# Optimization experiments

Hardware: AMD Instinct MI355X
Metric: run time of the kernel (lower is better)

The kernel has to match this reference:

```python
import jax, jax.numpy as jnp
import numpy as np

N_NODES = 100000
N_EDGES = 1600000
IN_FEATS = 128
HEADS = 4
OUT_FEATS = 32
NEG_SLOPE = 0.2


def setup_inputs() -> dict:
    key = jax.random.key(0)
    ks = jax.random.split(key, 7)
    x = jax.random.normal(ks[0], (N_NODES, IN_FEATS), dtype=jnp.float32)
    fc_w = jax.random.normal(ks[1], (HEADS * OUT_FEATS, IN_FEATS), dtype=jnp.float32) * (1.0 / np.sqrt(IN_FEATS))
    attn_l = jax.random.normal(ks[2], (HEADS, OUT_FEATS), dtype=jnp.float32) * (1.0 / np.sqrt(OUT_FEATS))
    attn_r = jax.random.normal(ks[3], (HEADS, OUT_FEATS), dtype=jnp.float32) * (1.0 / np.sqrt(OUT_FEATS))
    bias = jnp.zeros((HEADS * OUT_FEATS,), dtype=jnp.float32)
    src = jax.random.randint(ks[4], (N_EDGES,), 0, N_NODES, dtype=jnp.int64 if jax.config.jax_enable_x64 else jnp.int32)
    dst = jax.random.randint(ks[5], (N_EDGES,), 0, N_NODES, dtype=jnp.int64 if jax.config.jax_enable_x64 else jnp.int32)
    return {"x": x, "fc_w": fc_w, "attn_l": attn_l, "attn_r": attn_r, "bias": bias, "src": src, "dst": dst}


def reference(x, fc_w, attn_l, attn_r, bias, src, dst):
    """DGL GATConv (feat_drop=attn_drop=0, residual identity since in==H*D,
    allow_zero_in_degree=True, activation=None), then concat heads."""
    N = x.shape[0]
    H, D = attn_l.shape
    # linear projection: [N, H, D]
    feat = (x @ fc_w.T).reshape(N, H, D)
    # per-node attention halves: [N, H]
    el = jnp.einsum('nhd,hd->nh', feat, attn_l)
    er = jnp.einsum('nhd,hd->nh', feat, attn_r)
    # per-edge score with leaky relu: [E, H]
    e = el[src] + er[dst]
    e = jnp.where(e > 0, e, NEG_SLOPE * e)
    # edge softmax grouped by destination node
    emax = jax.ops.segment_max(e, dst, num_segments=N)          # [N, H]
    ee = jnp.exp(e - emax[dst])                                  # [E, H]
    denom = jax.ops.segment_sum(ee, dst, num_segments=N)        # [N, H]
    a = ee / jnp.maximum(denom[dst], jnp.float32(1e-38))         # [E, H]
    # weighted message + scatter aggregate: [N, H, D]
    msg = feat[src] * a[:, :, None]
    rst = jax.ops.segment_sum(msg, dst, num_segments=N)
    # residual (identity since in_feats == H*D) + bias
    rst = rst + x.reshape(N, H, D) + bias.reshape(1, H, D)
    # concat heads
    return rst.reshape(N, H * D)
```

## Files before the change

kernel.cpp:

```cpp
#include <hip/hip_runtime.h>
#include <math.h>

#define NEG_SLOPE 0.2f
#define PB 256
#define BKT_SHIFT 8
#define WSLICES 8

typedef __attribute__((ext_vector_type(8))) short bf16x8;
typedef __attribute__((ext_vector_type(4))) float f32x4;

__device__ __forceinline__ unsigned bf16_rne(float f) {
  unsigned u = __float_as_uint(f);
  return (u + 0x7fff + ((u >> 16) & 1)) >> 16;
}

__device__ __forceinline__ float lrelu_exp(float v) {
  v = v > 0.f ? v : NEG_SLOPE * v;
  return __expf(v);
}

__global__ void fc_conv(const float* __restrict__ fc_w,
                        unsigned* __restrict__ fc_wb, int n) {
  const int i = blockIdx.x * 256 + threadIdx.x;
  if (i < n) {
    const float2 v = reinterpret_cast<const float2*>(fc_w)[i];
    fc_wb[i] = bf16_rne(v.x) | (bf16_rne(v.y) << 16);
  }
}

__global__ __launch_bounds__(256) void gemm_feat_attn(
    const float* __restrict__ x, const unsigned* __restrict__ fc_wb,
    const float* __restrict__ attn_l, const float* __restrict__ attn_r,
    unsigned* __restrict__ featb, float* __restrict__ el,
    float* __restrict__ er, int N)
{
  __shared__ __align__(16) unsigned x_lds[64 * 68];
  __shared__ __align__(16) unsigned w_lds[128 * 68];
  const int t = threadIdx.x;
  const int row_base = blockIdx.x * 64;

  {
    const uint4* fb4 = reinterpret_cast<const uint4*>(fc_wb);
#pragma unroll
    for (int k = 0; k < 8; ++k) {
      const int i4 = t + k * 256;
      const uint4 v = fb4[i4];
      const int row = i4 >> 4;
      unsigned* d = &w_lds[row * 68 + (i4 & 15) * 4];
      d[0] = v.x; d[1] = v.y; d[2] = v.z; d[3] = v.w;
    }
  }
  {
    const int r = t >> 2, q = t & 3;
    const int grow = min(row_base + r, N - 1);
    const float* src = x + (size_t)grow * 128 + q * 32;
    unsigned* dstp = &x_lds[r * 68 + q * 16];
#pragma unroll
    for (int i = 0; i < 8; ++i) {
      const float4 v = *reinterpret_cast<const float4*>(src + i * 4);
      dstp[2 * i]     = bf16_rne(v.x) | (bf16_rne(v.y) << 16);
      dstp[2 * i + 1] = bf16_rne(v.z) | (bf16_rne(v.w) << 16);
    }
  }
  __syncthreads();

  const int w = t >> 6;
  const int l = t & 63;
  const int cl = l & 15;
  const int g = l >> 4;

  bf16x8 a_frag[4];
#pragma unroll
  for (int ks = 0; ks < 4; ++ks)
    a_frag[ks] = *reinterpret_cast<const bf16x8*>(
        &x_lds[(w * 16 + cl) * 68 + ks * 16 + g * 4]);

  f32x4 acc[8];
#pragma unroll
  for (int ct = 0; ct < 8; ++ct) acc[ct] = (f32x4){0.f, 0.f, 0.f, 0.f};

#pragma unroll
  for (int ct = 0; ct < 8; ++ct) {
#pragma unroll
    for (int ks = 0; ks < 4; ++ks) {
      const bf16x8 b_frag = *reinterpret_cast<const bf16x8*>(
          &w_lds[(ct * 16 + cl) * 68 + ks * 16 + g * 4]);
      acc[ct] = __builtin_amdgcn_mfma_f32_16x16x32_bf16(a_frag[ks], b_frag,
                                                        acc[ct], 0, 0, 0);
    }
  }

#pragma unroll
  for (int ct = 0; ct < 8; ++ct) {
#pragma unroll
    for (int r = 0; r < 4; ++r) {
      const float v = acc[ct][r];
      const float vn = __shfl_xor(v, 1);
      const int node = row_base + w * 16 + g * 4 + r;
      if ((cl & 1) == 0 && node < N) {
        featb[(size_t)node * 64 + ct * 8 + (cl >> 1)] =
            bf16_rne(v) | (bf16_rne(vn) << 16);
      }
    }
  }

  float al_lo[4], al_hi[4], ar_lo[4], ar_hi[4];
#pragma unroll
  for (int h = 0; h < 4; ++h) {
    al_lo[h] = attn_l[h * 32 + cl];
    al_hi[h] = attn_l[h * 32 + 16 + cl];
    ar_lo[h] = attn_r[h * 32 + cl];
    ar_hi[h] = attn_r[h * 32 + 16 + cl];
  }
#pragma unroll
  for (int r = 0; r < 4; ++r) {
    const int node = row_base + w * 16 + g * 4 + r;
#pragma unroll
    for (int h = 0; h < 4; ++h) {
      float pl = acc[2 * h][r] * al_lo[h] + acc[2 * h + 1][r] * al_hi[h];
      float pr = acc[2 * h][r] * ar_lo[h] + acc[2 * h + 1][r] * ar_hi[h];
#pragma unroll
      for (int d = 1; d < 16; d <<= 1) {
        pl += __shfl_xor(pl, d);
        pr += __shfl_xor(pr, d);
      }
      if (cl == 0 && node < N) {
        el[(size_t)node * 4 + h] = pl;
        er[(size_t)node * 4 + h] = pr;
      }
    }
  }
}

__global__ __launch_bounds__(256) void hist_bucket(const int* __restrict__ dst,
                                                   int* __restrict__ hist,
                                                   int E, int NB, int chunk) {
  __shared__ int h[512];
  const int k = blockIdx.x, t = threadIdx.x;
  for (int i = t; i < NB; i += 256) h[i] = 0;
  __syncthreads();
  const int beg = k * chunk, end = min(E, beg + chunk);
  for (int e = beg + t; e < end; e += 256)
    atomicAdd(&h[dst[e] >> BKT_SHIFT], 1);
  __syncthreads();
  for (int i = t; i < NB; i += 256) hist[i * PB + k] = h[i];
}

__global__ __launch_bounds__(256) void scan_a(const int* __restrict__ deg,
                                              int* __restrict__ offs,
                                              int* __restrict__ blk_sums,
                                              int n) {
  __shared__ int wsum[4];
  const int b = blockIdx.x, t = threadIdx.x;
  const int base = b * 2048 + t * 8;
  int v[8];
  int s = 0;
#pragma unroll
  for (int j = 0; j < 8; ++j) {
    v[j] = s;
    const int d = (base + j < n) ? deg[base + j] : 0;
    s += d;
  }
  const int lane = t & 63;
  int incl = s;
#pragma unroll
  for (int d = 1; d < 64; d <<= 1) {
    const int o = __shfl_up(incl, d);
    if (lane >= d) incl += o;
  }
  const int w = t >> 6;
  if (lane == 63) wsum[w] = incl;
  __syncthreads();
  int woff = 0;
  for (int ww = 0; ww < w; ++ww) woff += wsum[ww];
  const int thr_excl = woff + incl - s;
#pragma unroll
  for (int j = 0; j < 8; ++j)
    if (base + j < n) offs[base + j] = thr_excl + v[j];
  if (t == 255) blk_sums[b] = woff + incl;
}

__global__ void scan_b(const int* __restrict__ blk_sums,
                       int* __restrict__ blk_off, int* __restrict__ offs,
                       int n, int nb) {
  const int lane = threadIdx.x & 63;
  int v = (lane < nb) ? blk_sums[lane] : 0;
  int incl = v;
#pragma unroll
  for (int d = 1; d < 64; d <<= 1) {
    const int o = __shfl_up(incl, d);
    if (lane >= d) incl += o;
  }
  if (lane < nb) blk_off[lane] = incl - v;
  if (lane == 63) offs[n] = incl;
}

__global__ __launch_bounds__(256) void part_scatter(
    const int* __restrict__ src, const int* __restrict__ dst,
    const int* __restrict__ hscan, const int* __restrict__ blk_off,
    unsigned* __restrict__ part, int E, int NB, int chunk) {
  __shared__ int cur[512];
  const int k = blockIdx.x, t = threadIdx.x;
  for (int i = t; i < NB; i += 256) {
    const int m = i * PB + k;
    cur[i] = hscan[m] + blk_off[m >> 11];
  }
  __syncthreads();
  const int beg = k * chunk, end = min(E, beg + chunk);
  for (int e = beg + t; e < end; e += 256) {
    const int d = dst[e];
    const int b = d >> BKT_SHIFT;
    const int pos = atomicAdd(&cur[b], 1);
    part[pos] = (unsigned)src[e] |
                ((unsigned)(d & ((1 << BKT_SHIFT) - 1)) << 20);
  }
}

__global__ __launch_bounds__(256) void build_csr(
    const unsigned* __restrict__ part, const int* __restrict__ hscan,
    const int* __restrict__ blk_off, int* __restrict__ node_offs,
    unsigned* __restrict__ csr, int N, int E, int NB) {
  __shared__ int cnt[256];
  __shared__ int wtot[4];
  const int b = blockIdx.x, t = threadIdx.x;
  const int m0 = b * PB;
  const int bbase = hscan[m0] + blk_off[m0 >> 11];
  int bend = E;
  if (b + 1 < NB) {
    const int m1 = (b + 1) * PB;
    bend = hscan[m1] + blk_off[m1 >> 11];
  }
  const int node0 = b << BKT_SHIFT;
  cnt[t] = 0;
  __syncthreads();
  for (int p = bbase + t; p < bend; p += 256)
    atomicAdd(&cnt[part[p] >> 20], 1);
  __syncthreads();
  const int a0 = cnt[t];
  int incl = a0;
#pragma unroll
  for (int d1 = 1; d1 < 64; d1 <<= 1) {
    const int o = __shfl_up(incl, d1);
    if ((t & 63) >= d1) incl += o;
  }
  const int w = t >> 6;
  if ((t & 63) == 63) wtot[w] = incl;
  __syncthreads();
  int woff = 0;
  for (int ww = 0; ww < w; ++ww) woff += wtot[ww];
  const int e0 = woff + incl - a0;
  cnt[t] = e0;
  if (node0 + t < N) node_offs[node0 + t] = bbase + e0;
  if (b == NB - 1 && t == 0) node_offs[N] = E;
  __syncthreads();
  for (int p = bbase + t; p < bend; p += 256) {
    const unsigned v = part[p];
    const int lpos = atomicAdd(&cnt[v >> 20], 1);
    csr[bbase + lpos] = v;
  }
}

__global__ __launch_bounds__(256) void compute_w(
    const unsigned* __restrict__ csr, const int* __restrict__ hscan,
    const int* __restrict__ blk_off, const float* __restrict__ el,
    const float* __restrict__ er, float4* __restrict__ wsb, int E, int NB) {
  const int b = blockIdx.x / WSLICES;
  const int sl = blockIdx.x - b * WSLICES;
  const int m0 = b * PB;
  const int bbase = hscan[m0] + blk_off[m0 >> 11];
  int bend = E;
  if (b + 1 < NB) {
    const int m1 = (b + 1) * PB;
    bend = hscan[m1] + blk_off[m1 >> 11];
  }
  const int node0 = b << BKT_SHIFT;
  const int len = bend - bbase;
  const int per = (len + WSLICES - 1) / WSLICES;
  const int s0 = bbase + sl * per;
  const int s1 = min(bend, s0 + per);
  for (int pos = s0 + (int)threadIdx.x; pos < s1; pos += 256) {
    const unsigned v = csr[pos];
    const unsigned s = v & 0xFFFFFu;
    const unsigned ld = v >> 20;
    const float4 l4 = *reinterpret_cast<const float4*>(el + s * 4);
    const float4 r4 =
        *reinterpret_cast<const float4*>(er + (unsigned)(node0 + ld) * 4);
    float4 wv;
    wv.x = lrelu_exp(l4.x + r4.x);
    wv.y = lrelu_exp(l4.y + r4.y);
    wv.z = lrelu_exp(l4.z + r4.z);
    wv.w = lrelu_exp(l4.w + r4.w);
    wsb[pos] = wv;
  }
}

__global__ __launch_bounds__(256) void agg_kernel(
    const uint2* __restrict__ featb2, const unsigned* __restrict__ csr,
    const float* __restrict__ wf, const float* __restrict__ x,
    const float* __restrict__ bias, const int* __restrict__ node_offs,
    float* __restrict__ out, int N, int E)
{
  const int n = (int)((blockIdx.x * (size_t)blockDim.x + threadIdx.x) >> 6);
  if (n >= N) return;
  const unsigned lane = threadIdx.x & 63;
  const unsigned half = lane >> 5;
  const unsigned li = lane & 31;
  const unsigned hh = li >> 3;
  const int beg = node_offs[n];
  const int end = node_offs[n + 1];
  const int nfull = (end - beg) >> 3;

  float a0 = 0.f, a1 = 0.f, a2 = 0.f, a3 = 0.f, ds = 0.f;
  int p = beg;
  for (int gi = 0; gi < nfull; ++gi, p += 8) {
    unsigned pk[4]; float wv[4]; uint2 fv[4];
#pragma unroll
    for (int i = 0; i < 4; ++i) pk[i] = csr[(unsigned)p + 2 * i + half];
#pragma unroll
    for (int i = 0; i < 4; ++i)
      wv[i] = wf[((unsigned)p + 2 * i + half) * 4 + hh];
#pragma unroll
    for (int i = 0; i < 4; ++i)
      fv[i] = featb2[(pk[i] & 0xFFFFFu) * 32 + li];
#pragma unroll
    for (int i = 0; i < 4; ++i) {
      a0 = fmaf(wv[i], __uint_as_float(fv[i].x << 16), a0);
      a1 = fmaf(wv[i], __uint_as_float(fv[i].x & 0xffff0000u), a1);
      a2 = fmaf(wv[i], __uint_as_float(fv[i].y << 16), a2);
      a3 = fmaf(wv[i], __uint_as_float(fv[i].y & 0xffff0000u), a3);
      ds += wv[i];
    }
  }
  if (p < end) {
    const int last = end - 1;
#pragma unroll
    for (int i = 0; i < 4; ++i) {
      const int e = p + 2 * i + (int)half;
      const unsigned ec = (unsigned)min(e, last);
      const unsigned pk = csr[ec];
      float w = wf[ec * 4 + hh];
      if (e > last) w = 0.f;
      const uint2 fv = featb2[(pk & 0xFFFFFu) * 32 + li];
      a0 = fmaf(w, __uint_as_float(fv.x << 16), a0);
      a1 = fmaf(w, __uint_as_float(fv.x & 0xffff0000u), a1);
      a2 = fmaf(w, __uint_as_float(fv.y << 16), a2);
      a3 = fmaf(w, __uint_as_float(fv.y & 0xffff0000u), a3);
      ds += w;
    }
  }

  a0 += __shfl_xor(a0, 32);
  a1 += __shfl_xor(a1, 32);
  a2 += __shfl_xor(a2, 32);
  a3 += __shfl_xor(a3, 32);
  ds += __shfl_xor(ds, 32);

  if (half == 0) {
    const float inv = 1.f / fmaxf(ds, 1e-38f);
    const float4 xr = ((const float4*)x)[(unsigned)n * 32 + li];
    const float4 br = ((const float4*)bias)[li];
    float4 o;
    o.x = fmaf(a0, inv, xr.x + br.x);
    o.y = fmaf(a1, inv, xr.y + br.y);
    o.z = fmaf(a2, inv, xr.z + br.z);
    o.w = fmaf(a3, inv, xr.w + br.w);
    ((float4*)out)[(unsigned)n * 32 + li] = o;
  }
}

extern "C" void kernel_launch(void* const* d_in, const int* in_sizes, int n_in,
                              void* d_out, int out_size, void* d_ws,
                              size_t ws_size, hipStream_t stream) {
  const float* x      = (const float*)d_in[0];
  const float* fc_w   = (const float*)d_in[1];
  const float* attn_l = (const float*)d_in[2];
  const float* attn_r = (const float*)d_in[3];
  const float* bias   = (const float*)d_in[4];
  const int*   src    = (const int*)d_in[5];
  const int*   dst    = (const int*)d_in[6];
  const int N = in_sizes[0] / 128;
  const int E = in_sizes[5];
  float* out = (float*)d_out;

  const int NB = (N + 255) >> 8;
  const int M = NB * PB;
  const int chunk = (E + PB - 1) / PB;

  char* ws = (char*)d_ws;
  size_t off = 0;
  auto alloc = [&](size_t bytes) {
    void* p = ws + off;
    off += (bytes + 255) & ~(size_t)255;
    return p;
  };
  unsigned* featb   = (unsigned*)alloc((size_t)N * 128 * 2);
  unsigned* fc_wb   = (unsigned*)alloc(128 * 64 * 4);
  float* el         = (float*)alloc((size_t)N * 4 * 4);
  float* er         = (float*)alloc((size_t)N * 4 * 4);
  int*   hist       = (int*)alloc((size_t)M * 4);
  int*   hscan      = (int*)alloc((size_t)(M + 1) * 4);
  int*   node_offs  = (int*)alloc((size_t)(N + 1) * 4);
  int*   blk_sums   = (int*)alloc(256);
  int*   blk_off    = (int*)alloc(256);
  unsigned* part    = (unsigned*)alloc((size_t)E * 4);
  unsigned* csr     = (unsigned*)alloc((size_t)E * 4);
  float4* wsb       = (float4*)alloc((size_t)E * 16);

  fc_conv<<<32, 256, 0, stream>>>(fc_w, fc_wb, 128 * 64);
  gemm_feat_attn<<<(N + 63) / 64, 256, 0, stream>>>(x, fc_wb, attn_l, attn_r,
                                                    featb, el, er, N);
  hist_bucket<<<PB, 256, 0, stream>>>(dst, hist, E, NB, chunk);
  const int nb = (M + 2047) / 2048;
  scan_a<<<nb, 256, 0, stream>>>(hist, hscan, blk_sums, M);
  scan_b<<<1, 64, 0, stream>>>(blk_sums, blk_off, hscan, M, nb);
  part_scatter<<<PB, 256, 0, stream>>>(src, dst, hscan, blk_off, part, E, NB,
                                       chunk);
  build_csr<<<NB, 256, 0, stream>>>(part, hscan, blk_off, node_offs, csr, N,
                                    E, NB);
  compute_w<<<NB * WSLICES, 256, 0, stream>>>(csr, hscan, blk_off, el, er,
                                              wsb, E, NB);
  agg_kernel<<<(N + 3) / 4, 256, 0, stream>>>((const uint2*)featb, csr,
                                              (const float*)wsb, x, bias,
                                              node_offs, out, N, E);
}
```

Before: 170.1 us.

## Fold weight conversion into histogram, load GEMM A directly, unroll aggregation deeper

Folds the fc_w bf16 conversion into the hist_bucket kernel, which removes one kernel launch; hist_bucket now runs before the GEMM. The GEMM loads and converts its x fragments straight from global memory into registers, dropping the x LDS staging buffer, which lowers LDS use and may allow higher occupancy. The aggregation loop now processes 16 edges per iteration instead of 8, giving more gathers in flight, and the tail is restructured to match. In exchange it uses more registers, and short neighbour lists spend more of their work in the masked tail.

Result: faster. 163.1 us (-4.1%).

```diff
diff --git a/kernel.cpp b/kernel.cpp
--- a/kernel.cpp
+++ b/kernel.cpp
@@ -17,15 +17,6 @@
 __device__ __forceinline__ float lrelu_exp(float v) {
   v = v > 0.f ? v : NEG_SLOPE * v;
   return __expf(v);
-}
-
-__global__ void fc_conv(const float* __restrict__ fc_w,
-                        unsigned* __restrict__ fc_wb, int n) {
-  const int i = blockIdx.x * 256 + threadIdx.x;
-  if (i < n) {
-    const float2 v = reinterpret_cast<const float2*>(fc_w)[i];
-    fc_wb[i] = bf16_rne(v.x) | (bf16_rne(v.y) << 16);
-  }
 }
 
 __global__ __launch_bounds__(256) void gemm_feat_attn(
@@ -34,7 +25,6 @@
     unsigned* __restrict__ featb, float* __restrict__ el,
     float* __restrict__ er, int N)
 {
-  __shared__ __align__(16) unsigned x_lds[64 * 68];
   __shared__ __align__(16) unsigned w_lds[128 * 68];
   const int t = threadIdx.x;
   const int row_base = blockIdx.x * 64;
@@ -50,30 +40,28 @@
       d[0] = v.x; d[1] = v.y; d[2] = v.z; d[3] = v.w;
     }
   }
-  {
-    const int r = t >> 2, q = t & 3;
-    const int grow = min(row_base + r, N - 1);
-    const float* src = x + (size_t)grow * 128 + q * 32;
-    unsigned* dstp = &x_lds[r * 68 + q * 16];
-#pragma unroll
-    for (int i = 0; i < 8; ++i) {
-      const float4 v = *reinterpret_cast<const float4*>(src + i * 4);
-      dstp[2 * i]     = bf16_rne(v.x) | (bf16_rne(v.y) << 16);
-      dstp[2 * i + 1] = bf16_rne(v.z) | (bf16_rne(v.w) << 16);
-    }
-  }
-  __syncthreads();
 
   const int w = t >> 6;
   const int l = t & 63;
   const int cl = l & 15;
   const int g = l >> 4;
 
+  const int arow = min(row_base + w * 16 + cl, N - 1);
+  const float* __restrict__ xp = x + (size_t)arow * 128;
   bf16x8 a_frag[4];
 #pragma unroll
-  for (int ks = 0; ks < 4; ++ks)
-    a_frag[ks] = *reinterpret_cast<const bf16x8*>(
-        &x_lds[(w * 16 + cl) * 68 + ks * 16 + g * 4]);
+  for (int ks = 0; ks < 4; ++ks) {
+    const float4 v0 = *reinterpret_cast<const float4*>(xp + ks * 32 + g * 8);
+    const float4 v1 =
+        *reinterpret_cast<const float4*>(xp + ks * 32 + g * 8 + 4);
+    uint4 uu;
+    uu.x = bf16_rne(v0.x) | (bf16_rne(v0.y) << 16);
+    uu.y = bf16_rne(v0.z) | (bf16_rne(v0.w) << 16);
+    uu.z = bf16_rne(v1.x) | (bf16_rne(v1.y) << 16);
+    uu.w = bf16_rne(v1.z) | (bf16_rne(v1.w) << 16);
+    a_frag[ks] = *reinterpret_cast<bf16x8*>(&uu);
+  }
+  __syncthreads();
 
   f32x4 acc[8];
 #pragma unroll
@@ -134,9 +122,16 @@
 
 __global__ __launch_bounds__(256) void hist_bucket(const int* __restrict__ dst,
                                                    int* __restrict__ hist,
+                                                   const float* __restrict__ fc_w,
+                                                   unsigned* __restrict__ fc_wb,
                                                    int E, int NB, int chunk) {
   __shared__ int h[512];
   const int k = blockIdx.x, t = threadIdx.x;
+  if (k < 32) {
+    const int i = k * 256 + t;
+    const float2 v = reinterpret_cast<const float2*>(fc_w)[i];
+    fc_wb[i] = bf16_rne(v.x) | (bf16_rne(v.y) << 16);
+  }
   for (int i = t; i < NB; i += 256) h[i] = 0;
   __syncthreads();
   const int beg = k * chunk, end = min(E, beg + chunk);
@@ -308,22 +303,22 @@
   const unsigned hh = li >> 3;
   const int beg = node_offs[n];
   const int end = node_offs[n + 1];
-  const int nfull = (end - beg) >> 3;
+  const int nfull = (end - beg) >> 4;
 
   float a0 = 0.f, a1 = 0.f, a2 = 0.f, a3 = 0.f, ds = 0.f;
   int p = beg;
-  for (int gi = 0; gi < nfull; ++gi, p += 8) {
-    unsigned pk[4]; float wv[4]; uint2 fv[4];
-#pragma unroll
-    for (int i = 0; i < 4; ++i) pk[i] = csr[(unsigned)p + 2 * i + half];
-#pragma unroll
-    for (int i = 0; i < 4; ++i)
+  for (int gi = 0; gi < nfull; ++gi, p += 16) {
+    unsigned pk[8]; float wv[8]; uint2 fv[8];
+#pragma unroll
+    for (int i = 0; i < 8; ++i) pk[i] = csr[(unsigned)p + 2 * i + half];
+#pragma unroll
+    for (int i = 0; i < 8; ++i)
       wv[i] = wf[((unsigned)p + 2 * i + half) * 4 + hh];
 #pragma unroll
-    for (int i = 0; i < 4; ++i)
+    for (int i = 0; i < 8; ++i)
       fv[i] = featb2[(pk[i] & 0xFFFFFu) * 32 + li];
 #pragma unroll
-    for (int i = 0; i < 4; ++i) {
+    for (int i = 0; i < 8; ++i) {
       a0 = fmaf(wv[i], __uint_as_float(fv[i].x << 16), a0);
       a1 = fmaf(wv[i], __uint_as_float(fv[i].x & 0xffff0000u), a1);
       a2 = fmaf(wv[i], __uint_as_float(fv[i].y << 16), a2);
@@ -333,19 +328,25 @@
   }
   if (p < end) {
     const int last = end - 1;
-#pragma unroll
-    for (int i = 0; i < 4; ++i) {
-      const int e = p + 2 * i + (int)half;
-      const unsigned ec = (unsigned)min(e, last);
-      const unsigned pk = csr[ec];
-      float w = wf[ec * 4 + hh];
-      if (e > last) w = 0.f;
-      const uint2 fv = featb2[(pk & 0xFFFFFu) * 32 + li];
-      a0 = fmaf(w, __uint_as_float(fv.x << 16), a0);
-      a1 = fmaf(w, __uint_as_float(fv.x & 0xffff0000u), a1);
-      a2 = fmaf(w, __uint_as_float(fv.y << 16), a2);
-      a3 = fmaf(w, __uint_as_float(fv.y & 0xffff0000u), a3);
-      ds += w;
+    unsigned pk[8]; float wv[8]; uint2 fv[8]; int ee[8];
+#pragma unroll
+    for (int i = 0; i < 8; ++i) ee[i] = p + 2 * i + (int)half;
+#pragma unroll
+    for (int i = 0; i < 8; ++i) pk[i] = csr[(unsigned)min(ee[i], last)];
+#pragma unroll
+    for (int i = 0; i < 8; ++i)
+      wv[i] = wf[(unsigned)min(ee[i], last) * 4 + hh];
+#pragma unroll
+    for (int i = 0; i < 8; ++i)
+      fv[i] = featb2[(pk[i] & 0xFFFFFu) * 32 + li];
+#pragma unroll
+    for (int i = 0; i < 8; ++i) {
+      if (ee[i] > last) wv[i] = 0.f;
+      a0 = fmaf(wv[i], __uint_as_float(fv[i].x << 16), a0);
+      a1 = fmaf(wv[i], __uint_as_float(fv[i].x & 0xffff0000u), a1);
+      a2 = fmaf(wv[i], __uint_as_float(fv[i].y << 16), a2);
+      a3 = fmaf(wv[i], __uint_as_float(fv[i].y & 0xffff0000u), a3);
+      ds += wv[i];
     }
   }
 
@@ -406,10 +407,9 @@
   unsigned* csr     = (unsigned*)alloc((size_t)E * 4);
   float4* wsb       = (float4*)alloc((size_t)E * 16);
 
-  fc_conv<<<32, 256, 0, stream>>>(fc_w, fc_wb, 128 * 64);
+  hist_bucket<<<PB, 256, 0, stream>>>(dst, hist, fc_w, fc_wb, E, NB, chunk);
   gemm_feat_attn<<<(N + 63) / 64, 256, 0, stream>>>(x, fc_wb, attn_l, attn_r,
                                                     featb, el, er, N);
-  hist_bucket<<<PB, 256, 0, stream>>>(dst, hist, E, NB, chunk);
   const int nb = (M + 2047) / 2048;
   scan_a<<<nb, 256, 0, stream>>>(hist, hscan, blk_sums, M);
   scan_b<<<1, 64, 0, stream>>>(blk_sums, blk_off, hscan, M, nb);
```

## Fuse weight computation into CSR build, store bf16 weights, drop extra kernels

Applied to the files above, without the earlier changes.

Edge-weight computation moves into build_csr, which now uses 512 threads and writes bf16-packed weights next to the scatter, so the compute_w pass and its re-read of csr are gone. The fc_w bf16 conversion is folded into hist_bucket, and gemm reads x straight from global into MFMA fragments instead of staging it in LDS. agg_kernel reads 2-byte weights instead of 4-byte ones, halving that traffic. The cost is lower weight precision, and the fused scatter does its el/er gathers while holding the atomic path, which may reduce occupancy.

Measured after the change: 168.4 us. About the same (-1.0%).

```diff
diff --git a/kernel.cpp b/kernel.cpp
--- a/kernel.cpp
+++ b/kernel.cpp
@@ -4,7 +4,6 @@
 #define NEG_SLOPE 0.2f
 #define PB 256
 #define BKT_SHIFT 8
-#define WSLICES 8
 
 typedef __attribute__((ext_vector_type(8))) short bf16x8;
 typedef __attribute__((ext_vector_type(4))) float f32x4;
@@ -17,15 +16,6 @@
 __device__ __forceinline__ float lrelu_exp(float v) {
   v = v > 0.f ? v : NEG_SLOPE * v;
   return __expf(v);
-}
-
-__global__ void fc_conv(const float* __restrict__ fc_w,
-                        unsigned* __restrict__ fc_wb, int n) {
-  const int i = blockIdx.x * 256 + threadIdx.x;
-  if (i < n) {
-    const float2 v = reinterpret_cast<const float2*>(fc_w)[i];
-    fc_wb[i] = bf16_rne(v.x) | (bf16_rne(v.y) << 16);
-  }
 }
 
 __global__ __launch_bounds__(256) void gemm_feat_attn(
@@ -34,7 +24,6 @@
     unsigned* __restrict__ featb, float* __restrict__ el,
     float* __restrict__ er, int N)
 {
-  __shared__ __align__(16) unsigned x_lds[64 * 68];
   __shared__ __align__(16) unsigned w_lds[128 * 68];
   const int t = threadIdx.x;
   const int row_base = blockIdx.x * 64;
@@ -50,30 +39,28 @@
       d[0] = v.x; d[1] = v.y; d[2] = v.z; d[3] = v.w;
     }
   }
-  {
-    const int r = t >> 2, q = t & 3;
-    const int grow = min(row_base + r, N - 1);
-    const float* src = x + (size_t)grow * 128 + q * 32;
-    unsigned* dstp = &x_lds[r * 68 + q * 16];
-#pragma unroll
-    for (int i = 0; i < 8; ++i) {
-      const float4 v = *reinterpret_cast<const float4*>(src + i * 4);
-      dstp[2 * i]     = bf16_rne(v.x) | (bf16_rne(v.y) << 16);
-      dstp[2 * i + 1] = bf16_rne(v.z) | (bf16_rne(v.w) << 16);
-    }
-  }
-  __syncthreads();
 
   const int w = t >> 6;
   const int l = t & 63;
   const int cl = l & 15;
   const int g = l >> 4;
 
+  const int arow = min(row_base + w * 16 + cl, N - 1);
+  const float* __restrict__ xp = x + (size_t)arow * 128;
   bf16x8 a_frag[4];
 #pragma unroll
-  for (int ks = 0; ks < 4; ++ks)
-    a_frag[ks] = *reinterpret_cast<const bf16x8*>(
-        &x_lds[(w * 16 + cl) * 68 + ks * 16 + g * 4]);
+  for (int ks = 0; ks < 4; ++ks) {
+    const float4 v0 = *reinterpret_cast<const float4*>(xp + ks * 32 + g * 8);
+    const float4 v1 =
+        *reinterpret_cast<const float4*>(xp + ks * 32 + g * 8 + 4);
+    uint4 uu;
+    uu.x = bf16_rne(v0.x) | (bf16_rne(v0.y) << 16);
+    uu.y = bf16_rne(v0.z) | (bf16_rne(v0.w) << 16);
+    uu.z = bf16_rne(v1.x) | (bf16_rne(v1.y) << 16);
+    uu.w = bf16_rne(v1.z) | (bf16_rne(v1.w) << 16);
+    a_frag[ks] = *reinterpret_cast<bf16x8*>(&uu);
+  }
+  __syncthreads();
 
   f32x4 acc[8];
 #pragma unroll
@@ -134,9 +121,16 @@
 
 __global__ __launch_bounds__(256) void hist_bucket(const int* __restrict__ dst,
                                                    int* __restrict__ hist,
+                                                   const float* __restrict__ fc_w,
+                                                   unsigned* __restrict__ fc_wb,
                                                    int E, int NB, int chunk) {
   __shared__ int h[512];
   const int k = blockIdx.x, t = threadIdx.x;
+  if (k < 32) {
+    const int i = k * 256 + t;
+    const float2 v = reinterpret_cast<const float2*>(fc_w)[i];
+    fc_wb[i] = bf16_rne(v.x) | (bf16_rne(v.y) << 16);
+  }
   for (int i = t; i < NB; i += 256) h[i] = 0;
   __syncthreads();
   const int beg = k * chunk, end = min(E, beg + chunk);
@@ -216,10 +210,12 @@
   }
 }
 
-__global__ __launch_bounds__(256) void build_csr(
+__global__ __launch_bounds__(512) void build_csr(
     const unsigned* __restrict__ part, const int* __restrict__ hscan,
-    const int* __restrict__ blk_off, int* __restrict__ node_offs,
-    unsigned* __restrict__ csr, int N, int E, int NB) {
+    const int* __restrict__ blk_off, const float* __restrict__ el,
+    const float* __restrict__ er, int* __restrict__ node_offs,
+    unsigned* __restrict__ csr, uint2* __restrict__ wsb,
+    int N, int E, int NB) {
   __shared__ int cnt[256];
   __shared__ int wtot[4];
   const int b = blockIdx.x, t = threadIdx.x;
@@ -231,72 +227,55 @@
     bend = hscan[m1] + blk_off[m1 >> 11];
   }
   const int node0 = b << BKT_SHIFT;
-  cnt[t] = 0;
-  __syncthreads();
-  for (int p = bbase + t; p < bend; p += 256)
+  if (t < 256) cnt[t] = 0;
+  __syncthreads();
+  for (int p = bbase + t; p < bend; p += 512)
     atomicAdd(&cnt[part[p] >> 20], 1);
   __syncthreads();
-  const int a0 = cnt[t];
-  int incl = a0;
-#pragma unroll
-  for (int d1 = 1; d1 < 64; d1 <<= 1) {
-    const int o = __shfl_up(incl, d1);
-    if ((t & 63) >= d1) incl += o;
-  }
-  const int w = t >> 6;
-  if ((t & 63) == 63) wtot[w] = incl;
-  __syncthreads();
-  int woff = 0;
-  for (int ww = 0; ww < w; ++ww) woff += wtot[ww];
-  const int e0 = woff + incl - a0;
-  cnt[t] = e0;
-  if (node0 + t < N) node_offs[node0 + t] = bbase + e0;
-  if (b == NB - 1 && t == 0) node_offs[N] = E;
-  __syncthreads();
-  for (int p = bbase + t; p < bend; p += 256) {
+  int a0 = 0, incl = 0;
+  if (t < 256) {
+    a0 = cnt[t];
+    incl = a0;
+#pragma unroll
+    for (int d1 = 1; d1 < 64; d1 <<= 1) {
+      const int o = __shfl_up(incl, d1);
+      if ((t & 63) >= d1) incl += o;
+    }
+    if ((t & 63) == 63) wtot[t >> 6] = incl;
+  }
+  __syncthreads();
+  if (t < 256) {
+    const int w = t >> 6;
+    int woff = 0;
+    for (int ww = 0; ww < w; ++ww) woff += wtot[ww];
+    const int e0 = woff + incl - a0;
+    cnt[t] = e0;
+    if (node0 + t < N) node_offs[node0 + t] = bbase + e0;
+    if (b == NB - 1 && t == 0) node_offs[N] = E;
+  }
+  __syncthreads();
+  for (int p = bbase + t; p < bend; p += 512) {
     const unsigned v = part[p];
-    const int lpos = atomicAdd(&cnt[v >> 20], 1);
-    csr[bbase + lpos] = v;
-  }
-}
-
-__global__ __launch_bounds__(256) void compute_w(
-    const unsigned* __restrict__ csr, const int* __restrict__ hscan,
-    const int* __restrict__ blk_off, const float* __restrict__ el,
-    const float* __restrict__ er, float4* __restrict__ wsb, int E, int NB) {
-  const int b = blockIdx.x / WSLICES;
-  const int sl = blockIdx.x - b * WSLICES;
-  const int m0 = b * PB;
-  const int bbase = hscan[m0] + blk_off[m0 >> 11];
-  int bend = E;
-  if (b + 1 < NB) {
-    const int m1 = (b + 1) * PB;
-    bend = hscan[m1] + blk_off[m1 >> 11];
-  }
-  const int node0 = b << BKT_SHIFT;
-  const int len = bend - bbase;
-  const int per = (len + WSLICES - 1) / WSLICES;
-  const int s0 = bbase + sl * per;
-  const int s1 = min(bend, s0 + per);
-  for (int pos = s0 + (int)threadIdx.x; pos < s1; pos += 256) {
-    const unsigned v = csr[pos];
+    const unsigned ld = v >> 20;
     const unsigned s = v & 0xFFFFFu;
-    const unsigned ld = v >> 20;
+    const int lpos = atomicAdd(&cnt[ld], 1);
+    const int pos = bbase + lpos;
+    csr[pos] = v;
     const float4 l4 = *reinterpret_cast<const float4*>(el + s * 4);
     const float4 r4 =
         *reinterpret_cast<const float4*>(er + (unsigned)(node0 + ld) * 4);
-    float4 wv;
-    wv.x = lrelu_exp(l4.x + r4.x);
-    wv.y = lrelu_exp(l4.y + r4.y);
-    wv.z = lrelu_exp(l4.z + r4.z);
-    wv.w = lrelu_exp(l4.w + r4.w);
-    wsb[pos] = wv;
+    uint2 u;
+    u.x = bf16_rne(lrelu_exp(l4.x + r4.x)) |
+          (bf16_rne(lrelu_exp(l4.y + r4.y)) << 16);
+    u.y = bf16_rne(lrelu_exp(l4.z + r4.z)) |
+          (bf16_rne(lrelu_exp(l4.w + r4.w)) << 16);
+    wsb[pos] = u;
   }
 }
 
 __global__ __launch_bounds__(256) void agg_kernel(
     const uint2* __restrict__ featb2, const unsigned* __restrict__ csr,
-    const float* __restrict__ wf, const float* __restrict__ x,
+    const unsigned short* __restrict__ wsb_us, const float* __restrict__ x,
     const float* __restrict__ bias, const int* __restrict__ node_offs,
     float* __restrict__ out, int N, int E)
 {
@@ -306,6 +285,7 @@
   const unsigned half = lane >> 5;
   const unsigned li = lane & 31;
   const unsigned hh = li >> 3;
+  const unsigned short* __restrict__ wp = wsb_us + hh;
   const int beg = node_offs[n];
   const int end = node_offs[n + 1];
   const int nfull = (end - beg) >> 3;
@@ -313,22 +293,23 @@
   float a0 = 0.f, a1 = 0.f, a2 = 0.f, a3 = 0.f, ds = 0.f;
   int p = beg;
   for (int gi = 0; gi < nfull; ++gi, p += 8) {
-    unsigned pk[4]; float wv[4]; uint2 fv[4];
+    unsigned pk[4]; unsigned wu[4]; uint2 fv[4];
 #pragma unroll
     for (int i = 0; i < 4; ++i) pk[i] = csr[(unsigned)p + 2 * i + half];
 #pragma unroll
     for (int i = 0; i < 4; ++i)
-      wv[i] = wf[((unsigned)p + 2 * i + half) * 4 + hh];
+      wu[i] = wp[((unsigned)p + 2 * i + half) * 4];
 #pragma unroll
     for (int i = 0; i < 4; ++i)
       fv[i] = featb2[(pk[i] & 0xFFFFFu) * 32 + li];
 #pragma unroll
     for (int i = 0; i < 4; ++i) {
-      a0 = fmaf(wv[i], __uint_as_float(fv[i].x << 16), a0);
-      a1 = fmaf(wv[i], __uint_as_float(fv[i].x & 0xffff0000u), a1);
-      a2 = fmaf(wv[i], __uint_as_float(fv[i].y << 16), a2);
-      a3 = fmaf(wv[i], __uint_as_float(fv[i].y & 0xffff0000u), a3);
-      ds += wv[i];
+      const float w = __uint_as_float(wu[i] << 16);
+      a0 = fmaf(w, __uint_as_float(fv[i].x << 16), a0);
+      a1 = fmaf(w, __uint_as_float(fv[i].x & 0xffff0000u), a1);
+      a2 = fmaf(w, __uint_as_float(fv[i].y << 16), a2);
+      a3 = fmaf(w, __uint_as_float(fv[i].y & 0xffff0000u), a3);
+      ds += w;
     }
   }
   if (p < end) {
@@ -338,7 +319,7 @@
       const int e = p + 2 * i + (int)half;
       const unsigned ec = (unsigned)min(e, last);
       const unsigned pk = csr[ec];
-      float w = wf[ec * 4 + hh];
+      float w = __uint_as_float((unsigned)wp[ec * 4] << 16);
       if (e > last) w = 0.f;
       const uint2 fv = featb2[(pk & 0xFFFFFu) * 32 + li];
       a0 = fmaf(w, __uint_as_float(fv.x << 16), a0);
@@ -404,22 +385,19 @@
   int*   blk_off    = (int*)alloc(256);
   unsigned* part    = (unsigned*)alloc((size_t)E * 4);
   unsigned* csr     = (unsigned*)alloc((size_t)E * 4);
-  float4* wsb       = (float4*)alloc((size_t)E * 16);
-
-  fc_conv<<<32, 256, 0, stream>>>(fc_w, fc_wb, 128 * 64);
+  uint2* wsb        = (uint2*)alloc((size_t)E * 8);
+
+  hist_bucket<<<PB, 256, 0, stream>>>(dst, hist, fc_w, fc_wb, E, NB, chunk);
   gemm_feat_attn<<<(N + 63) / 64, 256, 0, stream>>>(x, fc_wb, attn_l, attn_r,
                                                     featb, el, er, N);
-  hist_bucket<<<PB, 256, 0, stream>>>(dst, hist, E, NB, chunk);
   const int nb = (M + 2047) / 2048;
   scan_a<<<nb, 256, 0, stream>>>(hist, hscan, blk_sums, M);
   scan_b<<<1, 64, 0, stream>>>(blk_sums, blk_off, hscan, M, nb);
   part_scatter<<<PB, 256, 0, stream>>>(src, dst, hscan, blk_off, part, E, NB,
                                        chunk);
-  build_csr<<<NB, 256, 0, stream>>>(part, hscan, blk_off, node_offs, csr, N,
-                                    E, NB);
-  compute_w<<<NB * WSLICES, 256, 0, stream>>>(csr, hscan, blk_off, el, er,
-                                              wsb, E, NB);
+  build_csr<<<NB, 512, 0, stream>>>(part, hscan, blk_off, el, er, node_offs,
+                                    csr, wsb, N, E, NB);
   agg_kernel<<<(N + 3) / 4, 256, 0, stream>>>((const uint2*)featb, csr,
-                                              (const float*)wsb, x, bias,
-                                              node_offs, out, N, E);
-}
+                                              (const unsigned short*)wsb, x,
+                                              bias, node_offs, out, N, E);
+}
```
